# Optimization experiments

Measured on AMD Instinct MI355X. Metric: run time of the kernel, lower is better.

## Reference

```python
import jax, jax.numpy as jnp
import numpy as np

N, E = 10000, 160000
IN_DIM, HID, EDGE_DIM = 512, 256, 51
EPS = 1e-8


def setup_inputs() -> dict:
    key = jax.random.key(0)
    ks = jax.random.split(key, 16)
    s = 0.02
    return {
        'h': jax.random.normal(ks[0], (N, IN_DIM), jnp.float32),
        'edge_index': jax.random.randint(ks[1], (2, E), 0, N, jnp.int64 if jax.config.jax_enable_x64 else jnp.int32),
        'edge_attr': jax.random.normal(ks[2], (E, EDGE_DIM), jnp.float32),
        'pos': jax.random.normal(ks[3], (N, 3), jnp.float32),
        # edge_mlp: Linear(2*IN_DIM+EDGE_DIM+1 -> HID), SiLU, Linear(HID -> HID), SiLU
        'eW1': jax.random.normal(ks[4], (2 * IN_DIM + EDGE_DIM + 1, HID), jnp.float32) * s,
        'eb1': jnp.zeros((HID,), jnp.float32),
        'eW2': jax.random.normal(ks[5], (HID, HID), jnp.float32) * s,
        'eb2': jnp.zeros((HID,), jnp.float32),
        # coord_mlp: Linear(HID->HID), SiLU, Linear(HID->1, no bias, tiny init)
        'cW1': jax.random.normal(ks[6], (HID, HID), jnp.float32) * s,
        'cb1': jnp.zeros((HID,), jnp.float32),
        'cW2': jax.random.normal(ks[7], (HID, 1), jnp.float32) * 0.001,
        # node_mlp: Linear(IN_DIM+HID -> HID), SiLU, Linear(HID -> HID)
        'nW1': jax.random.normal(ks[8], (IN_DIM + HID, HID), jnp.float32) * s,
        'nb1': jnp.zeros((HID,), jnp.float32),
        'nW2': jax.random.normal(ks[9], (HID, HID), jnp.float32) * s,
        'nb2': jnp.zeros((HID,), jnp.float32),
    }


def reference(h, edge_index, edge_attr, pos, eW1, eb1, eW2, eb2, cW1, cb1, cW2, nW1, nb1, nW2, nb2):
    row, col = edge_index[0], edge_index[1]
    diff = pos[row] - pos[col]                                   # [E,3]
    radial = jnp.sqrt(jnp.sum(diff * diff, axis=-1, keepdims=True)) + EPS  # [E,1]
    edge_in = jnp.concatenate([h[row], h[col], edge_attr, radial], axis=-1)  # [E,1076]
    e = jax.nn.silu(edge_in @ eW1 + eb1)
    e = jax.nn.silu(e @ eW2 + eb2)                               # [E,HID]
    coord_update = jax.nn.silu(e @ cW1 + cb1) @ cW2              # [E,1]
    coord_update = jnp.clip(coord_update, -1.0, 1.0)
    trans = coord_update * diff                                  # [E,3]
    agg_coord = jax.ops.segment_sum(trans, row, num_segments=pos.shape[0])
    pos_new = pos + agg_coord
    agg_node = jax.ops.segment_sum(e, row, num_segments=h.shape[0])  # [N,HID]
    h_new = jax.nn.silu(jnp.concatenate([h, agg_node], axis=-1) @ nW1 + nb1) @ nW2 + nb2
    # residual skipped: h_new last dim (HID=256) != h last dim (IN_DIM=512)
    return (h_new, pos_new)
```

## Files before the change

### kernel.cpp

```cpp
#include <hip/hip_runtime.h>
#include <hip/hip_bf16.h>

#define N_NODES 10000
#define N_PAD   10016
#define E_EDGES 160000
#define EB 32
#define NTILES (E_EDGES / EB)
#define HID 256

typedef __attribute__((ext_vector_type(4))) float f32x4;
typedef __attribute__((ext_vector_type(8))) short bf16x8;
typedef __attribute__((ext_vector_type(8))) unsigned short u16x8;
typedef __attribute__((ext_vector_type(4))) unsigned u32x4;
typedef unsigned short u16;
typedef __attribute__((address_space(1))) const unsigned int gu32;
typedef __attribute__((address_space(3))) unsigned int lu32;

__device__ __forceinline__ float silu_f(float x) { return x / (1.0f + __expf(-x)); }

__device__ __forceinline__ u16 f2bf(float f) {
    unsigned x = __float_as_uint(f);
    unsigned r = x + 0x7FFFu + ((x >> 16) & 1u);
    return (u16)(r >> 16);
}
__device__ __forceinline__ float bf2f(u16 u) {
    return __uint_as_float(((unsigned)u) << 16);
}
__device__ __forceinline__ unsigned cvtpk(float a, float b) {
    unsigned r;
    asm("v_cvt_pk_bf16_f32 %0, %1, %2" : "=v"(r) : "v"(a), "v"(b));
    return r;
}
__device__ __forceinline__ f32x4 mfma16(bf16x8 a, bf16x8 b, f32x4 c) {
    return __builtin_amdgcn_mfma_f32_16x16x32_bf16(a, b, c, 0, 0, 0);
}
__device__ __forceinline__ int actb(int row, int elem) {
    return (row * 512 + elem * 2) ^ ((row & 7) << 4);
}
__device__ __forceinline__ int xcd_swz(int bid, int nwg) {
    int qq = nwg >> 3, r8 = nwg & 7;
    int xcd = bid & 7, sub = bid >> 3;
    return (xcd < r8 ? xcd * (qq + 1) : r8 * (qq + 1) + (xcd - r8) * qq) + sub;
}

__global__ __launch_bounds__(256) void prep_weights(
    const float* __restrict__ eW1, const float* __restrict__ eW2,
    const float* __restrict__ cW1, const float* __restrict__ nW1,
    const float* __restrict__ nW2,
    u16* __restrict__ Wt3, u16* __restrict__ e1pt,
    u16* __restrict__ n1t, u16* __restrict__ n2t,
    u16* __restrict__ e2s, u16* __restrict__ c1s)
{
    const int y = blockIdx.y;
    if (y >= 6) {
        if (blockIdx.x >= 32) return;
        const float* W = (y == 6) ? eW2 : cW1;
        u16* dst = (y == 6) ? e2s : c1s;
        int T = blockIdx.x * 256 + threadIdx.x;
        int kc = T >> 10, rem = T & 1023;
        int q = rem >> 6, lane = rem & 63;
        int n = (q >> 2) * 64 + (q & 3) * 16 + (lane & 15);
        int kbase = kc * 32 + (lane >> 4) * 8;
        u16x8 o;
#pragma unroll
        for (int jj = 0; jj < 8; ++jj)
            o[jj] = f2bf(W[(size_t)(kbase + jj) * 256 + n]);
        *(u16x8*)&dst[(size_t)T * 8] = o;
        return;
    }
    const float* src; u16* dstp; int Ks, Kd;
    switch (y) {
        case 0: src = eW1;                dstp = Wt3;                Ks = 512; Kd = 512; break;
        case 1: src = eW1 + 512 * 256;    dstp = Wt3 + 256 * 512;    Ks = 512; Kd = 512; break;
        case 2: src = nW1;                dstp = Wt3 + 2 * 256 * 512; Ks = 512; Kd = 512; break;
        case 3: src = eW1 + 1024 * 256;   dstp = e1pt;               Ks = 52;  Kd = 64;  break;
        case 4: src = nW1 + 512 * 256;    dstp = n1t;                Ks = 256; Kd = 256; break;
        default: src = nW2;               dstp = n2t;                Ks = 256; Kd = 256; break;
    }
    int idx = blockIdx.x * 256 + threadIdx.x;
    if (idx < 256 * Kd) {
        int n = idx / Kd, k = idx - n * Kd;
        dstp[idx] = (k < Ks) ? f2bf(src[(size_t)k * 256 + n]) : (u16)0;
    }
}

__global__ __launch_bounds__(256) void conv_h(const float* __restrict__ h, u16* __restrict__ hb)
{
    size_t base = ((size_t)blockIdx.x * 256 + threadIdx.x) * 8;
    int row = (int)(base >> 9);
    u16x8 o;
    if (row < N_NODES) {
        const float4 f0 = *(const float4*)&h[base];
        const float4 f1 = *(const float4*)&h[base + 4];
        o[0] = f2bf(f0.x); o[1] = f2bf(f0.y); o[2] = f2bf(f0.z); o[3] = f2bf(f0.w);
        o[4] = f2bf(f1.x); o[5] = f2bf(f1.y); o[6] = f2bf(f1.z); o[7] = f2bf(f1.w);
    } else {
        o = (u16x8)0;
    }
    *(u16x8*)&hb[base] = o;
}

__global__ __launch_bounds__(256) void hist_kernel(const int* __restrict__ row,
                                                   int* __restrict__ hist)
{
    int e = blockIdx.x * 256 + threadIdx.x;
    if (e < E_EDGES) atomicAdd(&hist[row[e]], 1);
}

#define SCAN_PER 40
__global__ __launch_bounds__(256) void scan_kernel(const int* __restrict__ hist,
                                                   int* __restrict__ rowptr)
{
    __shared__ int a[256];
    const int t = threadIdx.x;
    const int base = t * SCAN_PER;
    int s = 0;
    for (int i = 0; i < SCAN_PER; ++i) {
        int b = base + i;
        if (b < N_PAD) s += hist[b];
    }
    a[t] = s;
    __syncthreads();
    for (int off = 1; off < 256; off <<= 1) {
        int v = (t >= off) ? a[t - off] : 0;
        __syncthreads();
        a[t] += v;
        __syncthreads();
    }
    int run = a[t] - s;
    for (int i = 0; i < SCAN_PER; ++i) {
        int b = base + i;
        if (b < N_PAD) { rowptr[b] = run; run += hist[b]; }
    }
    if (t == 255) rowptr[N_PAD] = a[255];
}

__global__ __launch_bounds__(256) void scatter_kernel(const int* __restrict__ row,
                                                      const int* __restrict__ rowptr,
                                                      int* __restrict__ cnt,
                                                      int* __restrict__ eorder)
{
    int e = blockIdx.x * 256 + threadIdx.x;
    if (e < E_EDGES) {
        int r = row[e];
        int p = rowptr[r] + atomicAdd(&cnt[r], 1);
        eorder[p] = e;
    }
}

__global__ __launch_bounds__(256) void precompute_X(
    const u16* __restrict__ hb, const u16* __restrict__ Wt3, u16* __restrict__ Xb)
{
    const int n0b = blockIdx.x * 32;
    const int which = blockIdx.y;
    const int j = threadIdx.x, wv = j >> 6, lane = j & 63;
    const int ml = lane & 15, g = lane >> 4;
    const int n0 = wv * 64;
    const u16* W = Wt3 + (size_t)which * 256 * 512;

    f32x4 acc[2][4];
    const f32x4 z = {0.f, 0.f, 0.f, 0.f};
#pragma unroll
    for (int mt = 0; mt < 2; ++mt)
#pragma unroll
        for (int nt = 0; nt < 4; ++nt) acc[mt][nt] = z;

    for (int kc = 0; kc < 16; ++kc) {
        bf16x8 a0 = *(const bf16x8*)&hb[(size_t)(n0b + ml) * 512 + kc * 32 + g * 8];
        bf16x8 a1 = *(const bf16x8*)&hb[(size_t)(n0b + 16 + ml) * 512 + kc * 32 + g * 8];
#pragma unroll
        for (int nt = 0; nt < 4; ++nt) {
            bf16x8 b = *(const bf16x8*)&W[(size_t)(n0 + nt * 16 + ml) * 512 + kc * 32 + g * 8];
            acc[0][nt] = mfma16(a0, b, acc[0][nt]);
            acc[1][nt] = mfma16(a1, b, acc[1][nt]);
        }
    }
#pragma unroll
    for (int mt = 0; mt < 2; ++mt)
#pragma unroll
        for (int nt = 0; nt < 4; ++nt) {
            int col = n0 + nt * 16 + ml;
#pragma unroll
            for (int i = 0; i < 4; ++i) {
                int row = n0b + mt * 16 + g * 4 + i;
                Xb[(size_t)row * 768 + which * 256 + col] = f2bf(acc[mt][nt][i]);
            }
        }
}

__global__ __launch_bounds__(256) void e1_kernel(
    const u16* __restrict__ Xb, const float* __restrict__ pos,
    const int* __restrict__ eidx, const float* __restrict__ eattr,
    const int* __restrict__ eorder,
    const u16* __restrict__ e1pt, const float* __restrict__ eb1,
    int t0, u16* __restrict__ act1s,
    int* __restrict__ ri_sorted, float* __restrict__ difp)
{
    __shared__ u16 attr[EB * 64];
    __shared__ u16 bufA[EB * 256];
    __shared__ int ri_s[EB], ci_s[EB], es_s[EB];
    __shared__ float rad_s[EB];

    const int j = threadIdx.x, w = j >> 6, lane = j & 63;
    const int ml = lane & 15, g = lane >> 4;
    const int n0 = w * 64;
    const f32x4 z = {0.f, 0.f, 0.f, 0.f};

    const int wg = xcd_swz(blockIdx.x, gridDim.x);
    const int e0 = (t0 + wg) * EB;

    if (j < EB) {
        int e = eorder[e0 + j];
        es_s[j] = e;
        int r = eidx[e], c = eidx[E_EDGES + e];
        ri_s[j] = r; ci_s[j] = c;
        ri_sorted[e0 + j] = r;
        float dx = pos[r * 3 + 0] - pos[c * 3 + 0];
        float dy = pos[r * 3 + 1] - pos[c * 3 + 1];
        float dz = pos[r * 3 + 2] - pos[c * 3 + 2];
        difp[e0 + j] = dx;
        difp[E_EDGES + e0 + j] = dy;
        difp[2 * E_EDGES + e0 + j] = dz;
        rad_s[j] = sqrtf(dx * dx + dy * dy + dz * dz) + 1e-8f;
    }
    __syncthreads();

#pragma unroll
    for (int t = 0; t < 4; ++t) {
        int li = t * 256 + j;
        int e = li >> 5, c = li & 31;
        const u16x8 xr = *(const u16x8*)&Xb[(size_t)ri_s[e] * 768 + c * 8];
        const u16x8 xc = *(const u16x8*)&Xb[(size_t)ci_s[e] * 768 + 256 + c * 8];
        u32x4 o;
#pragma unroll
        for (int k = 0; k < 4; ++k)
            o[k] = cvtpk(bf2f(xr[2 * k]) + bf2f(xc[2 * k]),
                         bf2f(xr[2 * k + 1]) + bf2f(xc[2 * k + 1]));
        *(u32x4*)((char*)bufA + ((e * 512 + c * 16) ^ ((e & 7) << 4))) = o;
    }
    for (int li = j; li < EB * 64; li += 256) {
        int row = li >> 6, k = li & 63;
        float v = (k < 51) ? eattr[(size_t)es_s[row] * 51 + k] : (k == 51 ? rad_s[row] : 0.f);
        int byte = (row * 128 + k * 2) ^ ((row & 7) << 4);
        attr[byte >> 1] = f2bf(v);
    }
    __syncthreads();

    f32x4 acc[2][4];
#pragma unroll
    for (int mt = 0; mt < 2; ++mt)
#pragma unroll
        for (int nt = 0; nt < 4; ++nt) acc[mt][nt] = z;
#pragma unroll
    for (int kc = 0; kc < 2; ++kc) {
        bf16x8 a0 = *(const bf16x8*)((const char*)attr + ((ml * 128 + (kc * 32 + g * 8) * 2) ^ ((ml & 7) << 4)));
        bf16x8 a1 = *(const bf16x8*)((const char*)attr + (((16 + ml) * 128 + (kc * 32 + g * 8) * 2) ^ ((ml & 7) << 4)));
#pragma unroll
        for (int nt = 0; nt < 4; ++nt) {
            bf16x8 b = *(const bf16x8*)&e1pt[(size_t)(n0 + nt * 16 + ml) * 64 + kc * 32 + g * 8];
            acc[0][nt] = mfma16(a0, b, acc[0][nt]);
            acc[1][nt] = mfma16(a1, b, acc[1][nt]);
        }
    }
#pragma unroll
    for (int nt = 0; nt < 4; ++nt) {
        int col = n0 + nt * 16 + ml;
        float b1 = eb1[col];
#pragma unroll
        for (int mt = 0; mt < 2; ++mt)
#pragma unroll
            for (int i = 0; i < 4; ++i) {
                int row = mt * 16 + g * 4 + i;
                int off = actb(row, col) >> 1;
                float v = acc[mt][nt][i] + b1 + bf2f(bufA[off]);
                bufA[off] = f2bf(silu_f(v));
            }
    }
    __syncthreads();

    const size_t obase = (size_t)wg * (EB * 256);
#pragma unroll
    for (int i = 0; i < 4; ++i) {
        int li = i * 256 + j;
        *(u16x8*)&act1s[obase + (size_t)li * 8] = *(const u16x8*)&bufA[li * 8];
    }
}

__global__ __launch_bounds__(256) void e2_kernel(
    const u16* __restrict__ act1s,
    const u16* __restrict__ e2s, const float* __restrict__ eb2,
    const u16* __restrict__ c1s, const float* __restrict__ cb1,
    const float* __restrict__ cW2,
    const int* __restrict__ ri_sorted, const float* __restrict__ difp,
    int t0, float* __restrict__ agg_node, float* __restrict__ agg_coord)
{
    __shared__ u16 bufA[EB * 256];
    __shared__ u16 ldsB[2][4096];
    __shared__ int ri_s[EB];
    __shared__ float red[EB * 4];

    const int j = threadIdx.x, w = j >> 6, lane = j & 63;
    const int ml = lane & 15, g = lane >> 4;
    const int n0 = w * 64;
    const f32x4 z = {0.f, 0.f, 0.f, 0.f};

    const int wg = xcd_swz(blockIdx.x, gridDim.x);
    const int e0 = (t0 + wg) * EB;

    {
        const size_t gbase = (size_t)wg * (EB * 256);
#pragma unroll
        for (int i = 0; i < 4; ++i) {
            const u16* src = act1s + gbase + (size_t)(i * 256 + j) * 8;
            u16* dst = &bufA[(i * 256 + j) * 8];
            __builtin_amdgcn_global_load_lds((gu32*)src, (lu32*)dst, 16, 0, 0);
        }
#pragma unroll
        for (int i = 0; i < 2; ++i) {
            const u16* src = e2s + (size_t)((4 * w + i) * 512 + lane * 8);
            u16* dst = &ldsB[0][w * 1024 + i * 512 + lane * 8];
            __builtin_amdgcn_global_load_lds((gu32*)src, (lu32*)dst, 16, 0, 0);
        }
    }
    if (j < EB) ri_s[j] = ri_sorted[e0 + j];
    asm volatile("s_waitcnt vmcnt(2) lgkmcnt(0)" ::: "memory");
    __builtin_amdgcn_s_barrier();

    f32x4 acc[2][4];

#pragma unroll
    for (int mt = 0; mt < 2; ++mt)
#pragma unroll
        for (int nt = 0; nt < 4; ++nt) acc[mt][nt] = z;
    for (int hc = 0; hc < 16; ++hc) {
        int kc = hc >> 1, h = hc & 1;
        if (hc < 15) {
            int kc1 = (hc + 1) >> 1, h1 = (hc + 1) & 1;
#pragma unroll
            for (int i = 0; i < 2; ++i) {
                const u16* src = e2s + (size_t)kc1 * 8192 + (4 * w + 2 * h1 + i) * 512 + lane * 8;
                u16* dst = &ldsB[(hc + 1) & 1][w * 1024 + i * 512 + lane * 8];
                __builtin_amdgcn_global_load_lds((gu32*)src, (lu32*)dst, 16, 0, 0);
            }
            asm volatile("s_waitcnt vmcnt(2)" ::: "memory");
        } else {
            asm volatile("s_waitcnt vmcnt(0)" ::: "memory");
        }
        __builtin_amdgcn_sched_barrier(0);
        bf16x8 a0 = *(const bf16x8*)((const char*)bufA + actb(ml, kc * 32 + g * 8));
        bf16x8 a1 = *(const bf16x8*)((const char*)bufA + actb(16 + ml, kc * 32 + g * 8));
#pragma unroll
        for (int i = 0; i < 2; ++i) {
            int nt = 2 * h + i;
            bf16x8 b = *(const bf16x8*)&ldsB[hc & 1][w * 1024 + i * 512 + lane * 8];
            acc[0][nt] = mfma16(a0, b, acc[0][nt]);
            acc[1][nt] = mfma16(a1, b, acc[1][nt]);
        }
    }
    asm volatile("s_waitcnt lgkmcnt(0)" ::: "memory");
    __builtin_amdgcn_s_barrier();

#pragma unroll
    for (int i = 0; i < 2; ++i) {
        const u16* src = c1s + (size_t)((4 * w + i) * 512 + lane * 8);
        u16* dst = &ldsB[0][w * 1024 + i * 512 + lane * 8];
        __builtin_amdgcn_global_load_lds((gu32*)src, (lu32*)dst, 16, 0, 0);
    }

#pragma unroll
    for (int nt = 0; nt < 4; ++nt) {
        int col = n0 + nt * 16 + ml;
        float b2 = eb2[col];
#pragma unroll
        for (int mt = 0; mt < 2; ++mt)
#pragma unroll
            for (int i = 0; i < 4; ++i) {
                int row = mt * 16 + g * 4 + i;
                bufA[actb(row, col) >> 1] = f2bf(silu_f(acc[mt][nt][i] + b2));
            }
    }
    asm volatile("s_waitcnt lgkmcnt(0)" ::: "memory");
    __builtin_amdgcn_s_barrier();

#pragma unroll
    for (int mt = 0; mt < 2; ++mt)
#pragma unroll
        for (int nt = 0; nt < 4; ++nt) acc[mt][nt] = z;
    for (int hc = 0; hc < 16; ++hc) {
        int kc = hc >> 1, h = hc & 1;
        if (hc < 15) {
            int kc1 = (hc + 1) >> 1, h1 = (hc + 1) & 1;
#pragma unroll
            for (int i = 0; i < 2; ++i) {
                const u16* src = c1s + (size_t)kc1 * 8192 + (4 * w + 2 * h1 + i) * 512 + lane * 8;
                u16* dst = &ldsB[(hc + 1) & 1][w * 1024 + i * 512 + lane * 8];
                __builtin_amdgcn_global_load_lds((gu32*)src, (lu32*)dst, 16, 0, 0);
            }
            asm volatile("s_waitcnt vmcnt(2)" ::: "memory");
        } else {
            asm volatile("s_waitcnt vmcnt(0)" ::: "memory");
        }
        __builtin_amdgcn_sched_barrier(0);
        bf16x8 a0 = *(const bf16x8*)((const char*)bufA + actb(ml, kc * 32 + g * 8));
        bf16x8 a1 = *(const bf16x8*)((const char*)bufA + actb(16 + ml, kc * 32 + g * 8));
#pragma unroll
        for (int i = 0; i < 2; ++i) {
            int nt = 2 * h + i;
            bf16x8 b = *(const bf16x8*)&ldsB[hc & 1][w * 1024 + i * 512 + lane * 8];
            acc[0][nt] = mfma16(a0, b, acc[0][nt]);
            acc[1][nt] = mfma16(a1, b, acc[1][nt]);
        }
    }

    float p[2][4] = {{0.f, 0.f, 0.f, 0.f}, {0.f, 0.f, 0.f, 0.f}};
#pragma unroll
    for (int nt = 0; nt < 4; ++nt) {
        int col = n0 + nt * 16 + ml;
        float b3 = cb1[col];
        float w2 = cW2[col];
#pragma unroll
        for (int mt = 0; mt < 2; ++mt)
#pragma unroll
            for (int i = 0; i < 4; ++i)
                p[mt][i] += silu_f(acc[mt][nt][i] + b3) * w2;
    }
#pragma unroll
    for (int mt = 0; mt < 2; ++mt)
#pragma unroll
        for (int i = 0; i < 4; ++i) {
            float v = p[mt][i];
            v += __shfl_xor(v, 1);
            v += __shfl_xor(v, 2);
            v += __shfl_xor(v, 4);
            v += __shfl_xor(v, 8);
            p[mt][i] = v;
        }
    if (ml == 0) {
#pragma unroll
        for (int mt = 0; mt < 2; ++mt)
#pragma unroll
            for (int i = 0; i < 4; ++i)
                red[(mt * 16 + g * 4 + i) * 4 + w] = p[mt][i];
    }
    __syncthreads();
    if (j < EB) {
        float u = red[j * 4 + 0] + red[j * 4 + 1] + red[j * 4 + 2] + red[j * 4 + 3];
        u = fminf(fmaxf(u, -1.f), 1.f);
        int rr = ri_s[j];
        atomicAdd(&agg_coord[(size_t)rr * 3 + 0], u * difp[e0 + j]);
        atomicAdd(&agg_coord[(size_t)rr * 3 + 1], u * difp[E_EDGES + e0 + j]);
        atomicAdd(&agg_coord[(size_t)rr * 3 + 2], u * difp[2 * E_EDGES + e0 + j]);
    }

    {
        float vreg[EB];
#pragma unroll
        for (int m = 0; m < EB; ++m)
            vreg[m] = bf2f(bufA[actb(m, j) >> 1]);
        int cur = ri_s[0];
        float s = vreg[0];
#pragma unroll
        for (int m = 1; m < EB; ++m) {
            int r = ri_s[m];
            if (r != cur) {
                atomicAdd(&agg_node[(size_t)cur * 256 + j], s);
                s = 0.f; cur = r;
            }
            s += vreg[m];
        }
        atomicAdd(&agg_node[(size_t)cur * 256 + j], s);
    }
}

__global__ __launch_bounds__(256) void node_kernel(
    const u16* __restrict__ Xb, const float* __restrict__ agg_node,
    const float* __restrict__ agg_coord, const float* __restrict__ pos,
    const u16* __restrict__ n1t, const float* __restrict__ nb1,
    const u16* __restrict__ n2t, const float* __restrict__ nb2,
    float* __restrict__ out)
{
    __shared__ u16 act1[32 * 256];
    __shared__ u16 act2[32 * 256];
    const int n0b = blockIdx.x * 32;
    const int j = threadIdx.x, wv = j >> 6, lane = j & 63;
    const int ml = lane & 15, g = lane >> 4;
    const int n0 = wv * 64;
    const f32x4 z = {0.f, 0.f, 0.f, 0.f};

    for (int li = j; li < 32 * 256; li += 256) {
        int r = li >> 8, c = li & 255;
        act1[actb(r, c) >> 1] = f2bf(agg_node[(size_t)(n0b + r) * 256 + c]);
    }
    __syncthreads();

    f32x4 acc[2][4];
#pragma unroll
    for (int mt = 0; mt < 2; ++mt)
#pragma unroll
        for (int nt = 0; nt < 4; ++nt) acc[mt][nt] = z;
    for (int kc = 0; kc < 8; ++kc) {
        bf16x8 a0 = *(const bf16x8*)((const char*)act1 + actb(ml, kc * 32 + g * 8));
        bf16x8 a1 = *(const bf16x8*)((const char*)act1 + actb(16 + ml, kc * 32 + g * 8));
#pragma unroll
        for (int nt = 0; nt < 4; ++nt) {
            bf16x8 b = *(const bf16x8*)&n1t[(size_t)(n0 + nt * 16 + ml) * 256 + kc * 32 + g * 8];
            acc[0][nt] = mfma16(a0, b, acc[0][nt]);
            acc[1][nt] = mfma16(a1, b, acc[1][nt]);
        }
    }
#pragma unroll
    for (int mt = 0; mt < 2; ++mt)
#pragma unroll
        for (int nt = 0; nt < 4; ++nt) {
            int col = n0 + nt * 16 + ml;
            float b1 = nb1[col];
#pragma unroll
            for (int i = 0; i < 4; ++i) {
                int m = mt * 16 + g * 4 + i;
                float v = acc[mt][nt][i] + b1 + bf2f(Xb[(size_t)(n0b + m) * 768 + 512 + col]);
                act2[actb(m, col) >> 1] = f2bf(silu_f(v));
            }
        }
    __syncthreads();
#pragma unroll
    for (int mt = 0; mt < 2; ++mt)
#pragma unroll
        for (int nt = 0; nt < 4; ++nt) acc[mt][nt] = z;
    for (int kc = 0; kc < 8; ++kc) {
        bf16x8 a0 = *(const bf16x8*)((const char*)act2 + actb(ml, kc * 32 + g * 8));
        bf16x8 a1 = *(const bf16x8*)((const char*)act2 + actb(16 + ml, kc * 32 + g * 8));
#pragma unroll
        for (int nt = 0; nt < 4; ++nt) {
            bf16x8 b = *(const bf16x8*)&n2t[(size_t)(n0 + nt * 16 + ml) * 256 + kc * 32 + g * 8];
            acc[0][nt] = mfma16(a0, b, acc[0][nt]);
            acc[1][nt] = mfma16(a1, b, acc[1][nt]);
        }
    }
#pragma unroll
    for (int mt = 0; mt < 2; ++mt)
#pragma unroll
        for (int nt = 0; nt < 4; ++nt) {
            int col = n0 + nt * 16 + ml;
            float b2 = nb2[col];
#pragma unroll
            for (int i = 0; i < 4; ++i) {
                int row = n0b + mt * 16 + g * 4 + i;
                if (row < N_NODES)
                    out[(size_t)row * 256 + col] = acc[mt][nt][i] + b2;
            }
        }
    if (j < 96) {
        int idx = n0b * 3 + j;
        if (idx < N_NODES * 3)
            out[(size_t)N_NODES * 256 + idx] = pos[idx] + agg_coord[idx];
    }
}

extern "C" void kernel_launch(void* const* d_in, const int* in_sizes, int n_in,
                              void* d_out, int out_size, void* d_ws, size_t ws_size,
                              hipStream_t stream)
{
    (void)in_sizes; (void)n_in; (void)out_size;
    const float* h     = (const float*)d_in[0];
    const int*   eidx  = (const int*)d_in[1];
    const float* eattr = (const float*)d_in[2];
    const float* pos   = (const float*)d_in[3];
    const float* eW1   = (const float*)d_in[4];
    const float* eb1   = (const float*)d_in[5];
    const float* eW2   = (const float*)d_in[6];
    const float* eb2   = (const float*)d_in[7];
    const float* cW1   = (const float*)d_in[8];
    const float* cb1   = (const float*)d_in[9];
    const float* cW2   = (const float*)d_in[10];
    const float* nW1   = (const float*)d_in[11];
    const float* nb1   = (const float*)d_in[12];
    const float* nW2   = (const float*)d_in[13];
    const float* nb2   = (const float*)d_in[14];
    float* out = (float*)d_out;

    u16* Xb   = (u16*)d_ws;
    u16* hb   = Xb + (size_t)N_PAD * 768;
    u16* Wt3  = hb + (size_t)N_PAD * 512;
    u16* e1pt = Wt3 + 3 * 256 * 512;
    u16* n1t  = e1pt + 256 * 64;
    u16* n2t  = n1t + 256 * 256;
    u16* e2s  = n2t + 256 * 256;
    u16* c1s  = e2s + 65536;
    float* agg_node  = (float*)(c1s + 65536);
    float* agg_coord = agg_node + (size_t)N_PAD * 256;
    int* hist   = (int*)(agg_coord + (size_t)N_PAD * 3);
    int* cnt    = hist + N_PAD;
    int* rowptr = cnt + N_PAD;
    int* eorder = rowptr + N_PAD + 1;
    int* ri_sorted = eorder + E_EDGES;
    float* difp = (float*)(ri_sorted + E_EDGES);
    char* wend = (char*)(difp + (size_t)3 * E_EDGES);
    u16* act1s = (u16*)(((uintptr_t)wend + 255) & ~(uintptr_t)255);

    size_t avail = ws_size - (size_t)((char*)act1s - (char*)d_ws);
    int tiles_cap = (int)(avail / (EB * 256 * sizeof(u16)));
    int chunk = tiles_cap < NTILES ? tiles_cap : NTILES;
    if (chunk < 1) chunk = 1;

    hipMemsetAsync(agg_node, 0, (size_t)N_PAD * 259 * sizeof(float), stream);
    hipMemsetAsync(hist, 0, (size_t)2 * N_PAD * sizeof(int), stream);

    prep_weights<<<dim3(512, 8), 256, 0, stream>>>(eW1, eW2, cW1, nW1, nW2,
                                                   Wt3, e1pt, n1t, n2t, e2s, c1s);
    conv_h<<<(N_PAD * 512 / 8) / 256, 256, 0, stream>>>(h, hb);

    hist_kernel<<<(E_EDGES + 255) / 256, 256, 0, stream>>>(eidx, hist);
    scan_kernel<<<1, 256, 0, stream>>>(hist, rowptr);
    scatter_kernel<<<(E_EDGES + 255) / 256, 256, 0, stream>>>(eidx, rowptr, cnt, eorder);

    precompute_X<<<dim3(N_PAD / 32, 3), 256, 0, stream>>>(hb, Wt3, Xb);

    for (int c = 0; c < NTILES; c += chunk) {
        int g = (NTILES - c) < chunk ? (NTILES - c) : chunk;
        e1_kernel<<<g, 256, 0, stream>>>(Xb, pos, eidx, eattr, eorder,
                                         e1pt, eb1, c, act1s, ri_sorted, difp);
        e2_kernel<<<g, 256, 0, stream>>>(act1s, e2s, eb2, c1s, cb1, cW2,
                                         ri_sorted, difp, c, agg_node, agg_coord);
    }

    node_kernel<<<N_PAD / 32, 256, 0, stream>>>(
        Xb, agg_node, agg_coord, pos, n1t, nb1, n2t, nb2, out);
}
```

Baseline: 313.4 us.

## Stage precompute_X operands in LDS with async loads and pre-convert edge attributes

```diff
diff --git a/kernel.cpp b/kernel.cpp
--- a/kernel.cpp
+++ b/kernel.cpp
@@ -47,15 +47,30 @@
     const float* __restrict__ eW1, const float* __restrict__ eW2,
     const float* __restrict__ cW1, const float* __restrict__ nW1,
     const float* __restrict__ nW2,
-    u16* __restrict__ Wt3, u16* __restrict__ e1pt,
-    u16* __restrict__ n1t, u16* __restrict__ n2t,
-    u16* __restrict__ e2s, u16* __restrict__ c1s)
+    u16* __restrict__ e1pt, u16* __restrict__ n1t, u16* __restrict__ n2t,
+    u16* __restrict__ e2s, u16* __restrict__ c1s, u16* __restrict__ w3c)
 {
     const int y = blockIdx.y;
-    if (y >= 6) {
+    if (y == 5) {
+        if (blockIdx.x >= 192) return;
+        int T = blockIdx.x * 256 + threadIdx.x;
+        int which = T >> 14, rem = T & 16383;
+        int kc = rem >> 10, rem2 = rem & 1023;
+        int q = rem2 >> 6, lane = rem2 & 63;
+        const float* W = (which == 0) ? eW1 : (which == 1) ? (eW1 + 512 * 256) : nW1;
+        int n = (q >> 2) * 64 + (q & 3) * 16 + (lane & 15);
+        int kbase = kc * 32 + (lane >> 4) * 8;
+        u16x8 o;
+#pragma unroll
+        for (int jj = 0; jj < 8; ++jj)
+            o[jj] = f2bf(W[(size_t)(kbase + jj) * 256 + n]);
+        *(u16x8*)&w3c[(size_t)T * 8] = o;
+        return;
+    }
+    if (y >= 3) {
         if (blockIdx.x >= 32) return;
-        const float* W = (y == 6) ? eW2 : cW1;
-        u16* dst = (y == 6) ? e2s : c1s;
+        const float* W = (y == 3) ? eW2 : cW1;
+        u16* dst = (y == 3) ? e2s : c1s;
         int T = blockIdx.x * 256 + threadIdx.x;
         int kc = T >> 10, rem = T & 1023;
         int q = rem >> 6, lane = rem & 63;
@@ -70,12 +85,9 @@
     }
     const float* src; u16* dstp; int Ks, Kd;
     switch (y) {
-        case 0: src = eW1;                dstp = Wt3;                Ks = 512; Kd = 512; break;
-        case 1: src = eW1 + 512 * 256;    dstp = Wt3 + 256 * 512;    Ks = 512; Kd = 512; break;
-        case 2: src = nW1;                dstp = Wt3 + 2 * 256 * 512; Ks = 512; Kd = 512; break;
-        case 3: src = eW1 + 1024 * 256;   dstp = e1pt;               Ks = 52;  Kd = 64;  break;
-        case 4: src = nW1 + 512 * 256;    dstp = n1t;                Ks = 256; Kd = 256; break;
-        default: src = nW2;               dstp = n2t;                Ks = 256; Kd = 256; break;
+        case 0: src = eW1 + 1024 * 256;  dstp = e1pt; Ks = 52;  Kd = 64;  break;
+        case 1: src = nW1 + 512 * 256;   dstp = n1t;  Ks = 256; Kd = 256; break;
+        default: src = nW2;              dstp = n2t;  Ks = 256; Kd = 256; break;
     }
     int idx = blockIdx.x * 256 + threadIdx.x;
     if (idx < 256 * Kd) {
@@ -100,6 +112,21 @@
     *(u16x8*)&hb[base] = o;
 }
 
+__global__ __launch_bounds__(256) void conv_attr(const float* __restrict__ eattr,
+                                                 u16* __restrict__ attrb)
+{
+    int T = blockIdx.x * 256 + threadIdx.x;
+    int row = T >> 3, ch = T & 7;
+    const float* src = eattr + (size_t)row * 51 + ch * 8;
+    u16x8 o;
+#pragma unroll
+    for (int t = 0; t < 8; ++t) {
+        int kk = ch * 8 + t;
+        o[t] = (kk < 51) ? f2bf(src[t]) : (u16)0;
+    }
+    *(u16x8*)&attrb[(size_t)T * 8] = o;
+}
+
 __global__ __launch_bounds__(256) void hist_kernel(const int* __restrict__ row,
                                                    int* __restrict__ hist)
 {
@@ -149,28 +176,62 @@
 }
 
 __global__ __launch_bounds__(256) void precompute_X(
-    const u16* __restrict__ hb, const u16* __restrict__ Wt3, u16* __restrict__ Xb)
-{
+    const u16* __restrict__ hb, const u16* __restrict__ w3c, u16* __restrict__ Xb)
+{
+    __shared__ u16 hs[32 * 512];
+    __shared__ u16 ldsB[2][4096];
+
     const int n0b = blockIdx.x * 32;
     const int which = blockIdx.y;
-    const int j = threadIdx.x, wv = j >> 6, lane = j & 63;
+    const int j = threadIdx.x, w = j >> 6, lane = j & 63;
     const int ml = lane & 15, g = lane >> 4;
-    const int n0 = wv * 64;
-    const u16* W = Wt3 + (size_t)which * 256 * 512;
+    const int n0 = w * 64;
+    const u16* Wc = w3c + (size_t)which * 16 * 8192;
+    const f32x4 z = {0.f, 0.f, 0.f, 0.f};
+
+#pragma unroll
+    for (int i = 0; i < 8; ++i) {
+        int d = i * 256 + j;
+        int row = d >> 6, c = d & 63;
+        const u16* src = &hb[(size_t)(n0b + row) * 512 + (c ^ (row & 7)) * 8];
+        __builtin_amdgcn_global_load_lds((gu32*)src, (lu32*)&hs[d * 8], 16, 0, 0);
+    }
+#pragma unroll
+    for (int i = 0; i < 2; ++i) {
+        const u16* src = Wc + (size_t)((4 * w + i) * 512 + lane * 8);
+        __builtin_amdgcn_global_load_lds((gu32*)src,
+            (lu32*)&ldsB[0][w * 1024 + i * 512 + lane * 8], 16, 0, 0);
+    }
+    asm volatile("s_waitcnt vmcnt(2) lgkmcnt(0)" ::: "memory");
+    __builtin_amdgcn_s_barrier();
 
     f32x4 acc[2][4];
-    const f32x4 z = {0.f, 0.f, 0.f, 0.f};
 #pragma unroll
     for (int mt = 0; mt < 2; ++mt)
 #pragma unroll
         for (int nt = 0; nt < 4; ++nt) acc[mt][nt] = z;
 
-    for (int kc = 0; kc < 16; ++kc) {
-        bf16x8 a0 = *(const bf16x8*)&hb[(size_t)(n0b + ml) * 512 + kc * 32 + g * 8];
-        bf16x8 a1 = *(const bf16x8*)&hb[(size_t)(n0b + 16 + ml) * 512 + kc * 32 + g * 8];
-#pragma unroll
-        for (int nt = 0; nt < 4; ++nt) {
-            bf16x8 b = *(const bf16x8*)&W[(size_t)(n0 + nt * 16 + ml) * 512 + kc * 32 + g * 8];
+    for (int hc = 0; hc < 32; ++hc) {
+        int kc = hc >> 1, h = hc & 1;
+        if (hc < 31) {
+            int kc1 = (hc + 1) >> 1, h1 = (hc + 1) & 1;
+#pragma unroll
+            for (int i = 0; i < 2; ++i) {
+                const u16* src = Wc + (size_t)kc1 * 8192 + (4 * w + 2 * h1 + i) * 512 + lane * 8;
+                __builtin_amdgcn_global_load_lds((gu32*)src,
+                    (lu32*)&ldsB[(hc + 1) & 1][w * 1024 + i * 512 + lane * 8], 16, 0, 0);
+            }
+            asm volatile("s_waitcnt vmcnt(2)" ::: "memory");
+        } else {
+            asm volatile("s_waitcnt vmcnt(0)" ::: "memory");
+        }
+        __builtin_amdgcn_sched_barrier(0);
+        bf16x8 a0 = *(const bf16x8*)((const char*)hs + ((ml * 1024 + (kc * 32 + g * 8) * 2) ^ ((ml & 7) << 4)));
+        bf16x8 a1 = *(const bf16x8*)((const char*)hs + (((16 + ml) * 1024 + (kc * 32 + g * 8) * 2) ^ ((ml & 7) << 4)));
+#pragma unroll
+        for (int i = 0; i < 2; ++i) {
+            int nt = 2 * h + i;
+            bf16x8 b = *(const bf16x8*)&ldsB[hc & 1][w * 1024 + i * 512 + lane * 8];
             acc[0][nt] = mfma16(a0, b, acc[0][nt]);
             acc[1][nt] = mfma16(a1, b, acc[1][nt]);
         }
@@ -190,7 +251,7 @@
 
 __global__ __launch_bounds__(256) void e1_kernel(
     const u16* __restrict__ Xb, const float* __restrict__ pos,
-    const int* __restrict__ eidx, const float* __restrict__ eattr,
+    const int* __restrict__ eidx, const u16* __restrict__ attrb,
     const int* __restrict__ eorder,
     const u16* __restrict__ e1pt, const float* __restrict__ eb1,
     int t0, u16* __restrict__ act1s,
@@ -238,11 +299,12 @@
                          bf2f(xr[2 * k + 1]) + bf2f(xc[2 * k + 1]));
         *(u32x4*)((char*)bufA + ((e * 512 + c * 16) ^ ((e & 7) << 4))) = o;
     }
-    for (int li = j; li < EB * 64; li += 256) {
-        int row = li >> 6, k = li & 63;
-        float v = (k < 51) ? eattr[(size_t)es_s[row] * 51 + k] : (k == 51 ? rad_s[row] : 0.f);
-        int byte = (row * 128 + k * 2) ^ ((row & 7) << 4);
-        attr[byte >> 1] = f2bf(v);
+    {
+        int row = j >> 3, g8 = j & 7;
+        u16x8 o = *(const u16x8*)&attrb[(size_t)es_s[row] * 64 + g8 * 8];
+        if (g8 == 6) o[3] = f2bf(rad_s[row]);
+        int byte = (row * 128 + g8 * 16) ^ ((row & 7) << 4);
+        *(u16x8*)((char*)attr + byte) = o;
     }
     __syncthreads();
 
@@ -580,13 +642,14 @@
 
     u16* Xb   = (u16*)d_ws;
     u16* hb   = Xb + (size_t)N_PAD * 768;
-    u16* Wt3  = hb + (size_t)N_PAD * 512;
-    u16* e1pt = Wt3 + 3 * 256 * 512;
+    u16* e1pt = hb + (size_t)N_PAD * 512;
     u16* n1t  = e1pt + 256 * 64;
     u16* n2t  = n1t + 256 * 256;
     u16* e2s  = n2t + 256 * 256;
     u16* c1s  = e2s + 65536;
-    float* agg_node  = (float*)(c1s + 65536);
+    u16* w3c  = c1s + 65536;
+    u16* attrb = w3c + 3 * 16 * 8192;
+    float* agg_node  = (float*)(attrb + (size_t)E_EDGES * 64);
     float* agg_coord = agg_node + (size_t)N_PAD * 256;
     int* hist   = (int*)(agg_coord + (size_t)N_PAD * 3);
     int* cnt    = hist + N_PAD;
@@ -605,19 +668,20 @@
     hipMemsetAsync(agg_node, 0, (size_t)N_PAD * 259 * sizeof(float), stream);
     hipMemsetAsync(hist, 0, (size_t)2 * N_PAD * sizeof(int), stream);
 
-    prep_weights<<<dim3(512, 8), 256, 0, stream>>>(eW1, eW2, cW1, nW1, nW2,
-                                                   Wt3, e1pt, n1t, n2t, e2s, c1s);
+    prep_weights<<<dim3(512, 6), 256, 0, stream>>>(eW1, eW2, cW1, nW1, nW2,
+                                                   e1pt, n1t, n2t, e2s, c1s, w3c);
     conv_h<<<(N_PAD * 512 / 8) / 256, 256, 0, stream>>>(h, hb);
+    conv_attr<<<(E_EDGES * 8) / 256, 256, 0, stream>>>(eattr, attrb);
 
     hist_kernel<<<(E_EDGES + 255) / 256, 256, 0, stream>>>(eidx, hist);
     scan_kernel<<<1, 256, 0, stream>>>(hist, rowptr);
     scatter_kernel<<<(E_EDGES + 255) / 256, 256, 0, stream>>>(eidx, rowptr, cnt, eorder);
 
-    precompute_X<<<dim3(N_PAD / 32, 3), 256, 0, stream>>>(hb, Wt3, Xb);
+    precompute_X<<<dim3(N_PAD / 32, 3), 256, 0, stream>>>(hb, w3c, Xb);
 
     for (int c = 0; c < NTILES; c += chunk) {
         int g = (NTILES - c) < chunk ? (NTILES - c) : chunk;
-        e1_kernel<<<g, 256, 0, stream>>>(Xb, pos, eidx, eattr, eorder,
+        e1_kernel<<<g, 256, 0, stream>>>(Xb, pos, eidx, attrb, eorder,
                                          e1pt, eb1, c, act1s, ri_sorted, difp);
         e2_kernel<<<g, 256, 0, stream>>>(act1s, e2s, eb2, c1s, cb1, cW2,
                                          ri_sorted, difp, c, agg_node, agg_coord);
```

Result: faster. 291.4 us (median of 2 runs) (-7.0%).
